# Optimization experiments

Hardware: AMD Instinct MI355X
Metric: run time of the kernel (lower is better)

The kernel has to match this reference:

```python
import jax, jax.numpy as jnp
from jax import lax
import numpy as np

POOLING_COUNTS = [15, 8, 8, 8]
N = 128          # segment_num
GROUPS = 4       # GroupNorm groups
TOPK = 5
NMS_THRESH = 0.5
EPS = 1e-5


def _build_structure(pooling_counts, n):
    """Static (numpy) replication of SparseMaxPool's mask2d and pooling schedule."""
    mask2d = np.zeros((n, n), dtype=bool)
    mask2d[np.arange(n), np.arange(n)] = True
    kinds = ['k2'] * pooling_counts[0]
    for c in pooling_counts[1:]:
        kinds += ['k3'] + ['k2'] * (c - 1)
    steps, stride, offset, k = [], 1, 0, 0
    for c in pooling_counts:
        for _ in range(c):
            offset += stride
            i = np.arange(0, n - offset, stride)
            j = np.arange(offset, n, stride)
            mask2d[i, j] = True
            steps.append((kinds[k], i, j))
            k += 1
        stride *= 2
    return mask2d, steps


_MASK2D, _STEPS = _build_structure(POOLING_COUNTS, N)


def sparse_max_pool(x):
    # x: [B, D, N] -> map2d: [B, D, N, N]
    B, D, _ = x.shape
    d = np.arange(N)
    map2d = jnp.zeros((B, D, N, N), x.dtype).at[:, :, d, d].set(x)
    for kind, i, j in _STEPS:
        if kind == 'k2':      # MaxPool1d(kernel=2, stride=1)
            x = jnp.maximum(x[..., :-1], x[..., 1:])
        else:                 # MaxPool1d(kernel=3, stride=2)
            m = jnp.maximum(jnp.maximum(x[..., :-2], x[..., 1:-1]), x[..., 2:])
            x = m[..., ::2]
        map2d = map2d.at[:, :, i, j].set(x)
    return map2d


def group_norm(x, gamma, beta):
    B, C, H, W = x.shape
    xg = x.reshape(B, GROUPS, C // GROUPS, H, W)
    mu = xg.mean(axis=(2, 3, 4), keepdims=True)
    var = xg.var(axis=(2, 3, 4), keepdims=True)
    xn = ((xg - mu) * lax.rsqrt(var + EPS)).reshape(B, C, H, W)
    return xn * gamma[None, :, None, None] + beta[None, :, None, None]


def decode(map2d, conv1_w, gn_gamma, gn_beta, conv2_w, conv2_b):
    dn = ('NCHW', 'OIHW', 'NCHW')
    h = lax.conv_general_dilated(map2d, conv1_w, (1, 1), [(1, 1), (1, 1)], dimension_numbers=dn)
    h = jax.nn.relu(group_norm(h, gn_gamma, gn_beta))
    out = lax.conv_general_dilated(h, conv2_w, (1, 1), [(0, 0), (0, 0)], dimension_numbers=dn)
    return out + conv2_b[None, :, None, None]


def greedy_nms(moments, scores):
    # moments: [M, 2] (start, end); scores: [M]
    M = moments.shape[0]
    order = jnp.argsort(-scores)
    m = moments[order]
    starts, ends = m[:, 0], m[:, 1]
    ar = jnp.arange(M)

    def body(i, sup):
        inter = jnp.clip(jnp.minimum(ends, ends[i]) - jnp.maximum(starts, starts[i]), 0.0)
        union = jnp.maximum(ends, ends[i]) - jnp.minimum(starts, starts[i])
        iou = inter / union
        newly = (iou > NMS_THRESH) & (ar > i) & jnp.logical_not(sup[i])
        return sup | newly

    sup = lax.fori_loop(0, M - 1, body, jnp.zeros((M,), bool))
    keep = jnp.logical_not(sup)
    # first TOPK kept rows in sorted order (static shape)
    pri = jnp.where(keep, M - ar, 0)
    _, idx = lax.top_k(pri, TOPK)
    return m[idx]


def reference(fea, duration, conv1_w, gn_gamma, gn_beta, conv2_w, conv2_b):
    map2d = sparse_max_pool(fea)
    out = decode(map2d, conv1_w, gn_gamma, gn_beta, conv2_w, conv2_b)
    mask = jnp.asarray(_MASK2D, out.dtype)
    score2d = (jax.nn.sigmoid(out) * mask)[0, 0]           # [N, N]
    # score2d_to_moments_scores: nonzero of masked map == static nonzero of mask2d
    gi, gj = np.nonzero(_MASK2D)                            # row-major, matches torch.nonzero
    scores = score2d[gi, gj]                                # [M]
    dur = float(duration)
    moments = jnp.asarray(
        np.stack([gi * (dur / N), (gj + 1) * (dur / N)], axis=-1), jnp.float32
    )                                                       # [M, 2]
    return greedy_nms(moments, scores)                      # [TOPK, 2]


def setup_inputs() -> dict:
    key = jax.random.key(0)
    k0, k1, k2 = jax.random.split(key, 3)
    D = 768
    return {
        'fea': jax.random.normal(k0, (1, D, N), jnp.float32),
        'duration': 30,
        'conv1_w': jax.random.normal(k1, (D, D, 3, 3), jnp.float32) * 0.02,
        'gn_gamma': jnp.ones((D,), jnp.float32),
        'gn_beta': jnp.zeros((D,), jnp.float32),
        'conv2_w': jax.random.normal(k2, (1, D, 1, 1), jnp.float32) * 0.02,
        'conv2_b': jnp.zeros((1,), jnp.float32),
    }
```

## Files before the change

### kernel.cpp

```cpp
#include <hip/hip_runtime.h>
#include <math.h>

#define NPIX 128
#define MASKM 2548
#define NPAD 2560
#define MG   6912
#define KD   768

typedef __attribute__((ext_vector_type(8))) short bf16x8;
typedef __attribute__((ext_vector_type(4))) float f32x4;
typedef __attribute__((ext_vector_type(16))) float f32x16;
typedef __attribute__((ext_vector_type(8))) unsigned short ushort8;

static constexpr size_t OFF_QI   = 0;
static constexpr size_t OFF_QJ   = OFF_QI + NPAD * 4;
static constexpr size_t OFF_QIDX = OFF_QJ + NPAD * 4;
static constexpr size_t OFF_APIX = OFF_QIDX + 16384 * 4;
static constexpr size_t OFF_START= OFF_APIX + 16384 * 4;
static constexpr size_t OFF_PART = OFF_START + 128 * 4;
static constexpr size_t OFF_STAT = OFF_PART + 512 * 8 * 8;
static constexpr size_t OFF_SC   = OFF_STAT + 256;
static constexpr size_t OFF_HM   = OFF_SC + NPAD * 4;
static constexpr size_t OFF_AH   = OFF_HM + (size_t)MASKM * KD * 4;
static constexpr size_t OFF_AL   = OFF_AH + (size_t)MG * KD * 2;
static constexpr size_t OFF_BH   = OFF_AL + (size_t)MG * KD * 2;
static constexpr size_t OFF_BL   = OFF_BH + (size_t)NPAD * KD * 2;
static constexpr size_t OFF_YT   = OFF_BL + (size_t)NPAD * KD * 2;
static constexpr size_t OFF_X    = OFF_YT;

__device__ __forceinline__ unsigned short f2bf(float f) {
    unsigned u = __float_as_uint(f);
    u = u + 0x7FFFu + ((u >> 16) & 1u);
    return (unsigned short)(u >> 16);
}
__device__ __forceinline__ float bf2f(unsigned short h) {
    return __uint_as_float(((unsigned)h) << 16);
}

__device__ __forceinline__ bool mask_allowed(int i, int d) {
    if (d == 0) return true;
    if (d <= 15) return true;
    if (d <= 31) return (d >= 17) && ((d & 1) == 1) && ((i & 1) == 0);
    if (d <= 63) return (d >= 35) && ((d & 3) == 3) && ((i & 3) == 0);
    return (d >= 71) && ((d & 7) == 7) && ((i & 7) == 0);
}
__device__ __forceinline__ bool masked_ij(int i, int j) {
    return (j >= i) && (j < NPIX) && (i >= 0) && mask_allowed(i, j - i);
}

__global__ void k_fill(int* __restrict__ qi, int* __restrict__ qj,
                       int* __restrict__ qidx, int* __restrict__ apix,
                       double* __restrict__ part) {
    __shared__ int cnt[NPIX];
    __shared__ int startv[NPIX];
    int tid = threadIdx.x;
    if (tid < NPIX) {
        int c = 0;
        for (int d = 0; tid + d < NPIX; ++d) if (mask_allowed(tid, d)) ++c;
        cnt[tid] = c;
    }
    __syncthreads();
    if (tid == 0) {
        int s = 0;
        for (int r = 0; r < NPIX; ++r) { startv[r] = s; s += cnt[r]; }
    }
    __syncthreads();
    int p = blockIdx.x * 256 + tid;
    int i = p >> 7, j = p & 127;
    int q = -1;
    if (masked_ij(i, j)) {
        int d = j - i, r = 0;
        for (int dd = 0; dd < d; ++dd) r += mask_allowed(i, dd) ? 1 : 0;
        q = startv[i] + r;
        qi[q] = i; qj[q] = j;
    }
    qidx[p] = q;
    int act = 0;
    #pragma unroll
    for (int dy = -1; dy <= 1; ++dy)
        #pragma unroll
        for (int dx = -1; dx <= 1; ++dx)
            if (masked_ij(i + dy, j + dx)) act = 1;
    apix[p] = act;
    if (blockIdx.x == 0 && tid < 8) part[tid] = 0.0;
}

__global__ void k_buildX(const float* __restrict__ fea, const int* __restrict__ qi,
                         const int* __restrict__ qj, float* __restrict__ X) {
    __shared__ float tab[8][NPIX];
    int c = blockIdx.x, t = threadIdx.x;
    tab[0][t] = fea[c * NPIX + t];
    __syncthreads();
    #pragma unroll
    for (int l = 1; l < 8; ++l) {
        int half = 1 << (l - 1), full = 1 << l;
        if (t + full <= NPIX) tab[l][t] = fmaxf(tab[l - 1][t], tab[l - 1][t + half]);
        __syncthreads();
    }
    #pragma unroll
    for (int it = 0; it < 20; ++it) {
        int q = it * 128 + t;
        float v = 0.f;
        if (q < MASKM) {
            int i = qi[q], j = qj[q];
            int len = j - i + 1;
            int l = 31 - __clz(len);
            v = fmaxf(tab[l][i], tab[l][j + 1 - (1 << l)]);
        }
        X[c * NPAD + q] = v;
    }
}

#define PASTR 148
__global__ __launch_bounds__(256) void k_prepA(const float* __restrict__ w1,
                                               unsigned short* __restrict__ Ah,
                                               unsigned short* __restrict__ Al) {
    __shared__ float tile[64 * PASTR];
    int co0 = blockIdx.x * 64, ci0 = blockIdx.y * 64;
    int tid = threadIdx.x;
    for (int s = 0; s < 4; ++s) {
        int cib = ci0 + s * 16;
        __syncthreads();
        for (int idx = tid; idx < 2304; idx += 256) {
            int row = idx / 36, c4 = idx % 36;
            float4 v = *(const float4*)(w1 + (size_t)(co0 + row) * MG + cib * 9 + c4 * 4);
            *(float4*)&tile[row * PASTR + c4 * 4] = v;
        }
        __syncthreads();
        for (int idx = tid; idx < 1152; idx += 256) {
            int tap = idx / 128;
            int rem = idx - tap * 128;
            int co = rem >> 1, half = rem & 1;
            ushort8 vh, vl;
            #pragma unroll
            for (int c = 0; c < 8; ++c) {
                float v = tile[co * PASTR + (half * 8 + c) * 9 + tap];
                unsigned short hi = f2bf(v);
                vh[c] = hi;
                vl[c] = f2bf(v - bf2f(hi));
            }
            size_t ob = (size_t)(tap * 768 + co0 + co) * KD + cib + half * 8;
            *(ushort8*)(Ah + ob) = vh;
            *(ushort8*)(Al + ob) = vl;
        }
    }
}

__global__ void k_trans(const float* __restrict__ src, int C,
                        unsigned short* __restrict__ dh, unsigned short* __restrict__ dl) {
    __shared__ float tile[64][65];
    int c0 = blockIdx.x * 64, k0 = blockIdx.y * 64;
    int t = threadIdx.x;
    int r = t >> 2, cq = (t & 3) << 4;
    const float* s = src + (size_t)(k0 + r) * C + c0 + cq;
    #pragma unroll
    for (int u = 0; u < 16; u += 4) {
        float4 v = *(const float4*)(s + u);
        tile[r][cq + u]     = v.x;
        tile[r][cq + u + 1] = v.y;
        tile[r][cq + u + 2] = v.z;
        tile[r][cq + u + 3] = v.w;
    }
    __syncthreads();
    size_t ob = (size_t)(c0 + r) * KD + k0 + cq;
    #pragma unroll
    for (int u = 0; u < 16; ++u) {
        float v = tile[cq + u][r];
        unsigned short hi = f2bf(v);
        float lo = v - bf2f(hi);
        dh[ob + u] = hi;
        dl[ob + u] = f2bf(lo);
    }
}

#define BUFSZ   73728
#define SB_BH   32768

__global__ __launch_bounds__(512, 1) void k_gemm(const unsigned short* __restrict__ Ah,
                                                 const unsigned short* __restrict__ Al,
                                                 const unsigned short* __restrict__ Bh,
                                                 const unsigned short* __restrict__ Bl,
                                                 float* __restrict__ Yt) {
    extern __shared__ char sm[];
    int tid = threadIdx.x;
    int wave = tid >> 6, lane = tid & 63;

    int bid = (int)blockIdx.x;
    int xcd = bid & 7, loc = bid >> 3;
    int m0 = loc * 256, n0 = xcd * 320;

    int wm = (wave & 3) << 6, wn = (wave >> 2) * 160;
    int r32 = lane & 31, hi2 = lane >> 5;
    int rb  = (r32 >> 4) * 1024 + hi2 * 256 + (r32 & 15) * 16;
    int awb = (wm >> 4) * 1024 + rb;
    int bwb = (wn >> 4) * 1024 + rb;

    int lrow = lane & 15, lchk = lane >> 4;
    const unsigned short* sp[9];
    int so[9];
    #pragma unroll
    for (int s = 0; s < 9; ++s) {
        int gid = wave * 9 + s;
        const unsigned short* base;
        int row0, ldso;
        if (gid < 16)      { base = Ah; row0 = m0 + gid * 16;        ldso = gid * 1024; }
        else if (gid < 32) { base = Al; row0 = m0 + (gid - 16) * 16; ldso = 16384 + (gid - 16) * 1024; }
        else if (gid < 52) { base = Bh; row0 = n0 + (gid - 32) * 16; ldso = SB_BH + (gid - 32) * 1024; }
        else               { base = Bl; row0 = n0 + (gid - 52) * 16; ldso = SB_BH + 20480 + (gid - 52) * 1024; }
        sp[s] = base + (size_t)(row0 + lrow) * KD + lchk * 8;
        so[s] = ldso;
    }

    f32x16 acc[2][5] = {};

    char* CB = sm;
    char* NB = sm + BUFSZ;

    #define STAGE(DST, s, koff) __builtin_amdgcn_global_load_lds( \
        (const __attribute__((address_space(1))) unsigned int*)(sp[s] + (koff)), \
        (__attribute__((address_space(3))) unsigned int*)((DST) + so[s]), 16, 0, 0)
    #define ARD(hl, mf, ks) (*(const bf16x8*)(CB + (hl) * 16384 + awb + (mf) * 2048 + (ks) * 512))
    #define BRD(hl, nf, ks) (*(const bf16x8*)(CB + SB_BH + (hl) * 20480 + bwb + (nf) * 2048 + (ks) * 512))
    #define TRIP(mf, nf, xh, xl, yh, yl) \
        acc[mf][nf] = __builtin_amdgcn_mfma_f32_32x32x16_bf16(xh, yh, acc[mf][nf], 0, 0, 0); \
        acc[mf][nf] = __builtin_amdgcn_mfma_f32_32x32x16_bf16(xh, yl, acc[mf][nf], 0, 0, 0); \
        acc[mf][nf] = __builtin_amdgcn_mfma_f32_32x32x16_bf16(xl, yh, acc[mf][nf], 0, 0, 0);

    #pragma unroll
    for (int s = 0; s < 9; ++s) STAGE(CB, s, 0);
    __syncthreads();

    for (int t = 0; t < 24; ++t) {
        int kn = (t + 1) * 32;
        if (t < 23) {
            #pragma unroll
            for (int s = 0; s < 9; ++s) STAGE(NB, s, kn);
        }
        #pragma unroll
        for (int ks = 0; ks < 2; ++ks) {
            bf16x8 a0h = ARD(0, 0, ks), a0l = ARD(1, 0, ks);
            bf16x8 a1h = ARD(0, 1, ks), a1l = ARD(1, 1, ks);
            bf16x8 bxh = BRD(0, 0, ks), bxl = BRD(1, 0, ks);
            bf16x8 byh = BRD(0, 1, ks), byl = BRD(1, 1, ks);
            __builtin_amdgcn_s_setprio(1);
            TRIP(0, 0, a0h, a0l, bxh, bxl)
            TRIP(1, 0, a1h, a1l, bxh, bxl)
            __builtin_amdgcn_s_setprio(0);
            bxh = BRD(0, 2, ks); bxl = BRD(1, 2, ks);
            __builtin_amdgcn_s_setprio(1);
            TRIP(0, 1, a0h, a0l, byh, byl)
            TRIP(1, 1, a1h, a1l, byh, byl)
            __builtin_amdgcn_s_setprio(0);
            byh = BRD(0, 3, ks); byl = BRD(1, 3, ks);
            __builtin_amdgcn_s_setprio(1);
            TRIP(0, 2, a0h, a0l, bxh, bxl)
            TRIP(1, 2, a1h, a1l, bxh, bxl)
            __builtin_amdgcn_s_setprio(0);
            bxh = BRD(0, 4, ks); bxl = BRD(1, 4, ks);
            __builtin_amdgcn_s_setprio(1);
            TRIP(0, 3, a0h, a0l, byh, byl)
            TRIP(1, 3, a1h, a1l, byh, byl)
            TRIP(0, 4, a0h, a0l, bxh, bxl)
            TRIP(1, 4, a1h, a1l, bxh, bxl)
            __builtin_amdgcn_s_setprio(0);
        }
        __syncthreads();
        char* tmp = CB; CB = NB; NB = tmp;
    }

    #pragma unroll
    for (int mf = 0; mf < 2; ++mf)
        #pragma unroll
        for (int nf = 0; nf < 5; ++nf) {
            int n = n0 + wn + nf * 32 + r32;
            size_t rowb = (size_t)n * MG + m0 + wm + mf * 32 + 4 * hi2;
            #pragma unroll
            for (int g = 0; g < 4; ++g) {
                f32x4 v = { acc[mf][nf][g * 4 + 0], acc[mf][nf][g * 4 + 1],
                            acc[mf][nf][g * 4 + 2], acc[mf][nf][g * 4 + 3] };
                *(f32x4*)(Yt + rowb + 8 * g) = v;
            }
        }
    #undef STAGE
    #undef ARD
    #undef BRD
    #undef TRIP
}

__global__ __launch_bounds__(256) void k_gather(const float* __restrict__ Yt,
                                                const int* __restrict__ qidx,
                                                const int* __restrict__ apix,
                                                float* __restrict__ hm,
                                                double* __restrict__ part) {
    __shared__ double red1[256 * 4], red2[256 * 4];
    int tid = threadIdx.x;
    int wave = tid >> 6, lane = tid & 63;
    double a1[3] = {0, 0, 0}, a2[3] = {0, 0, 0};
    int gs[3];
    #pragma unroll
    for (int s = 0; s < 3; ++s) gs[s] = (64 * s + lane) / 48;

    for (int it = 0; it < 8; ++it) {
        int p = blockIdx.x * 32 + wave * 8 + it;
        if (!apix[p]) continue;
        int y = p >> 7, x = p & 127;
        float4 hv[3] = {};
        #pragma unroll
        for (int tap = 0; tap < 9; ++tap) {
            int i = y + tap / 3 - 1, j = x + tap % 3 - 1;
            if ((unsigned)i < 128u && (unsigned)j < 128u) {
                int q = qidx[i * NPIX + j];
                if (q >= 0) {
                    const float* yr = Yt + (size_t)q * MG + tap * 768 + lane * 4;
                    #pragma unroll
                    for (int s = 0; s < 3; ++s) {
                        float4 v = *(const float4*)(yr + s * 256);
                        hv[s].x += v.x; hv[s].y += v.y; hv[s].z += v.z; hv[s].w += v.w;
                    }
                }
            }
        }
        int qp = qidx[p];
        if (qp >= 0) {
            #pragma unroll
            for (int s = 0; s < 3; ++s)
                *(float4*)(hm + (size_t)qp * KD + s * 256 + lane * 4) = hv[s];
        }
        #pragma unroll
        for (int s = 0; s < 3; ++s) {
            a1[s] += (double)hv[s].x + (double)hv[s].y + (double)hv[s].z + (double)hv[s].w;
            a2[s] += (double)hv[s].x * hv[s].x + (double)hv[s].y * hv[s].y +
                     (double)hv[s].z * hv[s].z + (double)hv[s].w * hv[s].w;
        }
    }
    #pragma unroll
    for (int g = 0; g < 4; ++g) { red1[tid * 4 + g] = 0.0; red2[tid * 4 + g] = 0.0; }
    #pragma unroll
    for (int s = 0; s < 3; ++s) { red1[tid * 4 + gs[s]] = a1[s]; red2[tid * 4 + gs[s]] = a2[s]; }
    __syncthreads();
    if (tid < 8) {
        int g = tid & 3;
        double s = 0.0;
        if (tid < 4) { for (int i = 0; i < 256; ++i) s += red1[i * 4 + g]; }
        else         { for (int i = 0; i < 256; ++i) s += red2[i * 4 + g]; }
        atomicAdd(&part[tid], s);
    }
}

__global__ void k_score(const float* __restrict__ hm, const double* __restrict__ part,
                        const float* __restrict__ gamma, const float* __restrict__ beta,
                        const float* __restrict__ w2, const float* __restrict__ b2,
                        float* __restrict__ scores) {
    int q = blockIdx.x * 4 + (threadIdx.x >> 6);
    int lane = threadIdx.x & 63;
    if (q >= MASKM) return;
    float mu[4], rs[4];
    const double cnt = 192.0 * 16384.0;
    #pragma unroll
    for (int g = 0; g < 4; ++g) {
        double m = part[g] / cnt;
        double v = part[4 + g] / cnt - m * m;
        mu[g] = (float)m;
        rs[g] = (float)(1.0 / sqrt(v + 1e-5));
    }
    const float* hp = hm + (size_t)q * KD;
    float s = 0.f;
    for (int c = lane; c < KD; c += 64) {
        int g = c / 192;
        float v = (hp[c] - mu[g]) * rs[g] * gamma[c] + beta[c];
        s += fmaxf(v, 0.f) * w2[c];
    }
    for (int o = 32; o; o >>= 1) s += __shfl_down(s, o, 64);
    if (lane == 0) scores[q] = 1.f / (1.f + expf(-(s + b2[0])));
}

__device__ __forceinline__ unsigned long long shfl_down_u64(unsigned long long v, int o) {
    unsigned lo = (unsigned)v, hi = (unsigned)(v >> 32);
    lo = __shfl_down(lo, o, 64);
    hi = __shfl_down(hi, o, 64);
    return ((unsigned long long)hi << 32) | lo;
}

__global__ void k_nms(const float* __restrict__ scores, const int* __restrict__ qi,
                      const int* __restrict__ qj, const int* __restrict__ durp,
                      float* __restrict__ out) {
    __shared__ unsigned long long key[MASKM];
    __shared__ float ss[MASKM], ee[MASKM];
    __shared__ unsigned char st[MASKM];
    __shared__ unsigned long long wm0[16], wm1[16];
    __shared__ int sh_keeper, keepq[5];
    __shared__ float sh_s0, sh_e0;
    int t = threadIdx.x;
    float delta = (float)(*durp) / 128.f;
    for (int i = t; i < MASKM; i += 1024) {
        unsigned sb = __float_as_uint(scores[i]);
        key[i] = ((unsigned long long)sb << 32) | (unsigned)(4095 - i);
        ss[i] = qi[i] * delta;
        ee[i] = (qj[i] + 1) * delta;
        st[i] = 0;
    }
    __syncthreads();
    for (int round = 0; round < 5; ++round) {
        unsigned long long b0 = 0, b1 = 0;
        for (int i = t; i < MASKM; i += 1024) {
            unsigned char s = st[i];
            unsigned long long k = key[i];
            if (s == 0) { if (k > b0) b0 = k; }
            else if (s == 1) { if (k > b1) b1 = k; }
        }
        for (int o = 32; o; o >>= 1) {
            unsigned long long u0 = shfl_down_u64(b0, o), u1 = shfl_down_u64(b1, o);
            if (u0 > b0) b0 = u0;
            if (u1 > b1) b1 = u1;
        }
        if ((t & 63) == 0) { wm0[t >> 6] = b0; wm1[t >> 6] = b1; }
        __syncthreads();
        if (t == 0) {
            unsigned long long B0 = 0, B1 = 0;
            for (int w = 0; w < 16; ++w) {
                if (wm0[w] > B0) B0 = wm0[w];
                if (wm1[w] > B1) B1 = wm1[w];
            }
            int keeper = (B0 != 0);
            unsigned long long B = keeper ? B0 : B1;
            int q = 4095 - (int)(B & 0xFFFFFFFFull);
            st[q] = keeper ? 2 : 3;
            sh_keeper = keeper;
            sh_s0 = ss[q]; sh_e0 = ee[q];
            keepq[round] = q;
        }
        __syncthreads();
        if (sh_keeper) {
            float s0 = sh_s0, e0 = sh_e0;
            for (int i = t; i < MASKM; i += 1024) {
                if (st[i] == 0) {
                    float inter = fminf(ee[i], e0) - fmaxf(ss[i], s0);
                    if (inter > 0.f) {
                        float uni = fmaxf(ee[i], e0) - fminf(ss[i], s0);
                        if (inter / uni > 0.5f) st[i] = 1;
                    }
                }
            }
        }
        __syncthreads();
    }
    if (t < 5) { out[t * 2] = ss[keepq[t]]; out[t * 2 + 1] = ee[keepq[t]]; }
}

extern "C" void kernel_launch(void* const* d_in, const int* in_sizes, int n_in,
                              void* d_out, int out_size, void* d_ws, size_t ws_size,
                              hipStream_t stream) {
    const float* fea   = (const float*)d_in[0];
    const int*   dur   = (const int*)d_in[1];
    const float* w1    = (const float*)d_in[2];
    const float* gamma = (const float*)d_in[3];
    const float* beta  = (const float*)d_in[4];
    const float* w2    = (const float*)d_in[5];
    const float* b2    = (const float*)d_in[6];
    float* out = (float*)d_out;

    char* ws = (char*)d_ws;
    int*    qi     = (int*)(ws + OFF_QI);
    int*    qj     = (int*)(ws + OFF_QJ);
    int*    qidx   = (int*)(ws + OFF_QIDX);
    int*    apix   = (int*)(ws + OFF_APIX);
    double* part   = (double*)(ws + OFF_PART);
    float*  scores = (float*)(ws + OFF_SC);
    float*  hm     = (float*)(ws + OFF_HM);
    unsigned short* AhU = (unsigned short*)(ws + OFF_AH);
    unsigned short* AlU = (unsigned short*)(ws + OFF_AL);
    unsigned short* BhU = (unsigned short*)(ws + OFF_BH);
    unsigned short* BlU = (unsigned short*)(ws + OFF_BL);
    float*  Yt     = (float*)(ws + OFF_YT);
    float*  X      = (float*)(ws + OFF_X);

    static bool gemm_attr_set = false;
    if (!gemm_attr_set) {
        hipFuncSetAttribute((const void*)k_gemm,
                            hipFuncAttributeMaxDynamicSharedMemorySize, 2 * BUFSZ);
        gemm_attr_set = true;
    }

    k_fill<<<64, 256, 0, stream>>>(qi, qj, qidx, apix, part);
    k_buildX<<<768, 128, 0, stream>>>(fea, qi, qj, X);
    k_prepA<<<dim3(12, 12), 256, 0, stream>>>(w1, AhU, AlU);
    k_trans<<<dim3(40, 12), 256, 0, stream>>>(X, NPAD, BhU, BlU);
    k_gemm<<<dim3(216), 512, 2 * BUFSZ, stream>>>(AhU, AlU, BhU, BlU, Yt);
    k_gather<<<512, 256, 0, stream>>>(Yt, qidx, apix, hm, part);
    k_score<<<637, 256, 0, stream>>>(hm, part, gamma, beta, w2, b2, scores);
    k_nms<<<1, 1024, 0, stream>>>(scores, qi, qj, dur, out);
}
```

Before: 279.5 us.

## Merge prep stages into one kernel and fuse gather/score/NMS with grid barriers

Folds the mask-index fill, sparse max-pool build, the B-matrix bf16 hi/lo split, and the weight split into one heterogeneous k_prep launch. The pooled features go straight into the transposed bf16 layout, which removes the intermediate X buffer and the separate transpose pass. The gather, GroupNorm/score and NMS stages become one persistent k_fused kernel that uses atomic grid-wide barriers, replacing three launches and their gaps. The barriers assume all 512 blocks are co-resident (3 per CU), which is a deadlock risk if occupancy falls short.

```diff
diff --git a/kernel.cpp b/kernel.cpp
--- a/kernel.cpp
+++ b/kernel.cpp
@@ -6,6 +6,7 @@
 #define NPAD 2560
 #define MG   6912
 #define KD   768
+#define FUSED_GRID 512
 
 typedef __attribute__((ext_vector_type(8))) short bf16x8;
 typedef __attribute__((ext_vector_type(4))) float f32x4;
@@ -16,17 +17,15 @@
 static constexpr size_t OFF_QJ   = OFF_QI + NPAD * 4;
 static constexpr size_t OFF_QIDX = OFF_QJ + NPAD * 4;
 static constexpr size_t OFF_APIX = OFF_QIDX + 16384 * 4;
-static constexpr size_t OFF_START= OFF_APIX + 16384 * 4;
-static constexpr size_t OFF_PART = OFF_START + 128 * 4;
-static constexpr size_t OFF_STAT = OFF_PART + 512 * 8 * 8;
-static constexpr size_t OFF_SC   = OFF_STAT + 256;
+static constexpr size_t OFF_BAR  = OFF_APIX + 16384 * 4;
+static constexpr size_t OFF_PART = OFF_BAR + 128 * 4;
+static constexpr size_t OFF_SC   = OFF_PART + 512 * 8 * 8;
 static constexpr size_t OFF_HM   = OFF_SC + NPAD * 4;
 static constexpr size_t OFF_AH   = OFF_HM + (size_t)MASKM * KD * 4;
 static constexpr size_t OFF_AL   = OFF_AH + (size_t)MG * KD * 2;
 static constexpr size_t OFF_BH   = OFF_AL + (size_t)MG * KD * 2;
 static constexpr size_t OFF_BL   = OFF_BH + (size_t)NPAD * KD * 2;
 static constexpr size_t OFF_YT   = OFF_BL + (size_t)NPAD * KD * 2;
-static constexpr size_t OFF_X    = OFF_YT;
 
 __device__ __forceinline__ unsigned short f2bf(float f) {
     unsigned u = __float_as_uint(f);
@@ -48,128 +47,168 @@
     return (j >= i) && (j < NPIX) && (i >= 0) && mask_allowed(i, j - i);
 }
 
-__global__ void k_fill(int* __restrict__ qi, int* __restrict__ qj,
-                       int* __restrict__ qidx, int* __restrict__ apix,
-                       double* __restrict__ part) {
-    __shared__ int cnt[NPIX];
-    __shared__ int startv[NPIX];
+__device__ __forceinline__ int rank_to_d(int i, int r) {
+    int rem = NPIX - i;
+    int c1 = rem < 16 ? rem : 16;
+    if (r < c1) return r;
+    r -= c1;
+    int h2 = (rem - 1) < 31 ? (rem - 1) : 31;
+    int c2 = (((i & 1) == 0) && h2 >= 17) ? ((h2 - 17) >> 1) + 1 : 0;
+    if (r < c2) return 17 + 2 * r;
+    r -= c2;
+    int h3 = (rem - 1) < 63 ? (rem - 1) : 63;
+    int c3 = (((i & 3) == 0) && h3 >= 35) ? ((h3 - 35) >> 2) + 1 : 0;
+    if (r < c3) return 35 + 4 * r;
+    r -= c3;
+    return 71 + 8 * r;
+}
+
+#define PREP_LDS 66816
+#define PASTR 148
+
+__global__ __launch_bounds__(256) void k_prep(const float* __restrict__ fea,
+                                              const float* __restrict__ w1,
+                                              int* __restrict__ qi, int* __restrict__ qj,
+                                              int* __restrict__ qidx, int* __restrict__ apix,
+                                              double* __restrict__ part, int* __restrict__ bar,
+                                              unsigned short* __restrict__ Ah,
+                                              unsigned short* __restrict__ Al,
+                                              unsigned short* __restrict__ Bh,
+                                              unsigned short* __restrict__ Bl) {
+    extern __shared__ char smp[];
     int tid = threadIdx.x;
-    if (tid < NPIX) {
-        int c = 0;
-        for (int d = 0; tid + d < NPIX; ++d) if (mask_allowed(tid, d)) ++c;
-        cnt[tid] = c;
-    }
-    __syncthreads();
-    if (tid == 0) {
-        int s = 0;
-        for (int r = 0; r < NPIX; ++r) { startv[r] = s; s += cnt[r]; }
-    }
-    __syncthreads();
-    int p = blockIdx.x * 256 + tid;
-    int i = p >> 7, j = p & 127;
-    int q = -1;
-    if (masked_ij(i, j)) {
-        int d = j - i, r = 0;
-        for (int dd = 0; dd < d; ++dd) r += mask_allowed(i, dd) ? 1 : 0;
-        q = startv[i] + r;
-        qi[q] = i; qj[q] = j;
-    }
-    qidx[p] = q;
-    int act = 0;
-    #pragma unroll
-    for (int dy = -1; dy <= 1; ++dy)
-        #pragma unroll
-        for (int dx = -1; dx <= 1; ++dx)
-            if (masked_ij(i + dy, j + dx)) act = 1;
-    apix[p] = act;
-    if (blockIdx.x == 0 && tid < 8) part[tid] = 0.0;
-}
-
-__global__ void k_buildX(const float* __restrict__ fea, const int* __restrict__ qi,
-                         const int* __restrict__ qj, float* __restrict__ X) {
-    __shared__ float tab[8][NPIX];
-    int c = blockIdx.x, t = threadIdx.x;
-    tab[0][t] = fea[c * NPIX + t];
-    __syncthreads();
-    #pragma unroll
-    for (int l = 1; l < 8; ++l) {
-        int half = 1 << (l - 1), full = 1 << l;
-        if (t + full <= NPIX) tab[l][t] = fmaxf(tab[l - 1][t], tab[l - 1][t + half]);
-        __syncthreads();
-    }
-    #pragma unroll
-    for (int it = 0; it < 20; ++it) {
-        int q = it * 128 + t;
-        float v = 0.f;
-        if (q < MASKM) {
-            int i = qi[q], j = qj[q];
-            int len = j - i + 1;
-            int l = 31 - __clz(len);
-            v = fmaxf(tab[l][i], tab[l][j + 1 - (1 << l)]);
-        }
-        X[c * NPAD + q] = v;
-    }
-}
-
-#define PASTR 148
-__global__ __launch_bounds__(256) void k_prepA(const float* __restrict__ w1,
-                                               unsigned short* __restrict__ Ah,
-                                               unsigned short* __restrict__ Al) {
-    __shared__ float tile[64 * PASTR];
-    int co0 = blockIdx.x * 64, ci0 = blockIdx.y * 64;
-    int tid = threadIdx.x;
-    for (int s = 0; s < 4; ++s) {
-        int cib = ci0 + s * 16;
-        __syncthreads();
-        for (int idx = tid; idx < 2304; idx += 256) {
-            int row = idx / 36, c4 = idx % 36;
-            float4 v = *(const float4*)(w1 + (size_t)(co0 + row) * MG + cib * 9 + c4 * 4);
-            *(float4*)&tile[row * PASTR + c4 * 4] = v;
-        }
-        __syncthreads();
-        for (int idx = tid; idx < 1152; idx += 256) {
-            int tap = idx / 128;
-            int rem = idx - tap * 128;
-            int co = rem >> 1, half = rem & 1;
-            ushort8 vh, vl;
+    int bid = blockIdx.x;
+
+    if (bid < 64) {
+        int* cnt = (int*)smp;
+        int* startv = cnt + NPIX;
+        if (tid < NPIX) {
+            int c = 0;
+            for (int d = 0; tid + d < NPIX; ++d) if (mask_allowed(tid, d)) ++c;
+            cnt[tid] = c;
+        }
+        __syncthreads();
+        if (tid == 0) {
+            int s = 0;
+            for (int r = 0; r < NPIX; ++r) { startv[r] = s; s += cnt[r]; }
+        }
+        __syncthreads();
+        int p = bid * 256 + tid;
+        int i = p >> 7, j = p & 127;
+        int q = -1;
+        if (masked_ij(i, j)) {
+            int d = j - i, r = 0;
+            for (int dd = 0; dd < d; ++dd) r += mask_allowed(i, dd) ? 1 : 0;
+            q = startv[i] + r;
+            qi[q] = i; qj[q] = j;
+        }
+        qidx[p] = q;
+        int act = 0;
+        #pragma unroll
+        for (int dy = -1; dy <= 1; ++dy)
             #pragma unroll
-            for (int c = 0; c < 8; ++c) {
-                float v = tile[co * PASTR + (half * 8 + c) * 9 + tap];
-                unsigned short hi = f2bf(v);
-                vh[c] = hi;
-                vl[c] = f2bf(v - bf2f(hi));
-            }
-            size_t ob = (size_t)(tap * 768 + co0 + co) * KD + cib + half * 8;
-            *(ushort8*)(Ah + ob) = vh;
-            *(ushort8*)(Al + ob) = vl;
-        }
-    }
-}
-
-__global__ void k_trans(const float* __restrict__ src, int C,
-                        unsigned short* __restrict__ dh, unsigned short* __restrict__ dl) {
-    __shared__ float tile[64][65];
-    int c0 = blockIdx.x * 64, k0 = blockIdx.y * 64;
-    int t = threadIdx.x;
-    int r = t >> 2, cq = (t & 3) << 4;
-    const float* s = src + (size_t)(k0 + r) * C + c0 + cq;
-    #pragma unroll
-    for (int u = 0; u < 16; u += 4) {
-        float4 v = *(const float4*)(s + u);
-        tile[r][cq + u]     = v.x;
-        tile[r][cq + u + 1] = v.y;
-        tile[r][cq + u + 2] = v.z;
-        tile[r][cq + u + 3] = v.w;
-    }
-    __syncthreads();
-    size_t ob = (size_t)(c0 + r) * KD + k0 + cq;
-    #pragma unroll
-    for (int u = 0; u < 16; ++u) {
-        float v = tile[cq + u][r];
-        unsigned short hi = f2bf(v);
-        float lo = v - bf2f(hi);
-        dh[ob + u] = hi;
-        dl[ob + u] = f2bf(lo);
+            for (int dx = -1; dx <= 1; ++dx)
+                if (masked_ij(i + dy, j + dx)) act = 1;
+        apix[p] = act;
+        if (bid == 0) {
+            if (tid < 8) part[tid] = 0.0;
+            if (tid == 8) bar[0] = 0;
+            if (tid == 9) bar[1] = 0;
+        }
+    } else if (bid < 112) {
+        float* tab = (float*)smp;
+        int* cnt = (int*)(smp + 65536);
+        int* startv = (int*)(smp + 66048);
+        int cb = bid - 64, c0 = cb * 16;
+        if (tid < NPIX) {
+            int c = 0;
+            for (int d = 0; tid + d < NPIX; ++d) if (mask_allowed(tid, d)) ++c;
+            cnt[tid] = c;
+        }
+        __syncthreads();
+        if (tid == 0) {
+            int s = 0;
+            for (int r = 0; r < NPIX; ++r) { startv[r] = s; s += cnt[r]; }
+            startv[NPIX] = s;
+        }
+        for (int idx = tid; idx < 16 * NPIX; idx += 256) {
+            int c = idx >> 7, x = idx & 127;
+            tab[(c * 8) * 128 + x] = fea[(size_t)(c0 + c) * NPIX + x];
+        }
+        __syncthreads();
+        for (int lvl = 1; lvl < 8; ++lvl) {
+            int half = 1 << (lvl - 1), full = 1 << lvl;
+            for (int idx = tid; idx < 16 * NPIX; idx += 256) {
+                int c = idx >> 7, x = idx & 127;
+                if (x + full <= NPIX)
+                    tab[(c * 8 + lvl) * 128 + x] =
+                        fmaxf(tab[(c * 8 + lvl - 1) * 128 + x],
+                              tab[(c * 8 + lvl - 1) * 128 + x + half]);
+            }
+            __syncthreads();
+        }
+        for (int q = tid; q < NPAD; q += 256) {
+            ushort8 vh0 = {}, vh1 = {}, vl0 = {}, vl1 = {};
+            if (q < MASKM) {
+                int i = 0;
+                #pragma unroll
+                for (int s = 64; s >= 1; s >>= 1) {
+                    int cand = i + s;
+                    if (cand <= 127 && startv[cand] <= q) i = cand;
+                }
+                int d = rank_to_d(i, q - startv[i]);
+                int j = i + d;
+                int len = d + 1;
+                int lvl = 31 - __clz(len);
+                int x2 = j + 1 - (1 << lvl);
+                #pragma unroll
+                for (int c = 0; c < 8; ++c) {
+                    float v = fmaxf(tab[(c * 8 + lvl) * 128 + i], tab[(c * 8 + lvl) * 128 + x2]);
+                    unsigned short hh = f2bf(v);
+                    vh0[c] = hh; vl0[c] = f2bf(v - bf2f(hh));
+                }
+                #pragma unroll
+                for (int c = 0; c < 8; ++c) {
+                    float v = fmaxf(tab[((c + 8) * 8 + lvl) * 128 + i], tab[((c + 8) * 8 + lvl) * 128 + x2]);
+                    unsigned short hh = f2bf(v);
+                    vh1[c] = hh; vl1[c] = f2bf(v - bf2f(hh));
+                }
+            }
+            *(ushort8*)(Bh + (size_t)q * KD + c0)     = vh0;
+            *(ushort8*)(Bh + (size_t)q * KD + c0 + 8) = vh1;
+            *(ushort8*)(Bl + (size_t)q * KD + c0)     = vl0;
+            *(ushort8*)(Bl + (size_t)q * KD + c0 + 8) = vl1;
+        }
+    } else {
+        float* tile = (float*)smp;
+        int pb = bid - 112;
+        int co0 = (pb % 12) * 64, ci0 = (pb / 12) * 64;
+        for (int s = 0; s < 4; ++s) {
+            int cib = ci0 + s * 16;
+            __syncthreads();
+            for (int idx = tid; idx < 2304; idx += 256) {
+                int row = idx / 36, c4 = idx % 36;
+                float4 v = *(const float4*)(w1 + (size_t)(co0 + row) * MG + cib * 9 + c4 * 4);
+                *(float4*)&tile[row * PASTR + c4 * 4] = v;
+            }
+            __syncthreads();
+            for (int idx = tid; idx < 1152; idx += 256) {
+                int tap = idx / 128;
+                int rem = idx - tap * 128;
+                int co = rem >> 1, half = rem & 1;
+                ushort8 vh, vl;
+                #pragma unroll
+                for (int c = 0; c < 8; ++c) {
+                    float v = tile[co * PASTR + (half * 8 + c) * 9 + tap];
+                    unsigned short hi = f2bf(v);
+                    vh[c] = hi;
+                    vl[c] = f2bf(v - bf2f(hi));
+                }
+                size_t ob = (size_t)(tap * 768 + co0 + co) * KD + cib + half * 8;
+                *(ushort8*)(Ah + ob) = vh;
+                *(ushort8*)(Al + ob) = vl;
+            }
+        }
     }
 }
 
@@ -212,7 +251,6 @@
     }
 
     f32x16 acc[2][5] = {};
-
     char* CB = sm;
     char* NB = sm + BUFSZ;
 
@@ -287,164 +325,206 @@
     #undef TRIP
 }
 
-__global__ __launch_bounds__(256) void k_gather(const float* __restrict__ Yt,
-                                                const int* __restrict__ qidx,
-                                                const int* __restrict__ apix,
-                                                float* __restrict__ hm,
-                                                double* __restrict__ part) {
-    __shared__ double red1[256 * 4], red2[256 * 4];
+#define FUSED_LDS 44544
+
+__device__ __forceinline__ void grid_arrive_wait(int* ctr) {
+    __threadfence();
+    __syncthreads();
+    if (threadIdx.x == 0) {
+        __hip_atomic_fetch_add(ctr, 1, __ATOMIC_RELEASE, __HIP_MEMORY_SCOPE_AGENT);
+        while (__hip_atomic_load(ctr, __ATOMIC_ACQUIRE, __HIP_MEMORY_SCOPE_AGENT) < FUSED_GRID)
+            __builtin_amdgcn_s_sleep(1);
+    }
+    __syncthreads();
+    __threadfence();
+}
+
+__global__ __launch_bounds__(256, 3) void k_fused(const float* __restrict__ Yt,
+                                                  const int* __restrict__ qidx,
+                                                  const int* __restrict__ apix,
+                                                  const int* __restrict__ qi,
+                                                  const int* __restrict__ qj,
+                                                  const int* __restrict__ durp,
+                                                  double* __restrict__ part,
+                                                  int* __restrict__ bar,
+                                                  float* __restrict__ hm,
+                                                  float* __restrict__ scores,
+                                                  const float* __restrict__ gamma,
+                                                  const float* __restrict__ beta,
+                                                  const float* __restrict__ w2,
+                                                  const float* __restrict__ b2,
+                                                  float* __restrict__ out) {
+    extern __shared__ char smf[];
     int tid = threadIdx.x;
+    int bid = (int)blockIdx.x;
     int wave = tid >> 6, lane = tid & 63;
-    double a1[3] = {0, 0, 0}, a2[3] = {0, 0, 0};
-    int gs[3];
-    #pragma unroll
-    for (int s = 0; s < 3; ++s) gs[s] = (64 * s + lane) / 48;
-
-    for (int it = 0; it < 8; ++it) {
-        int p = blockIdx.x * 32 + wave * 8 + it;
-        if (!apix[p]) continue;
-        int y = p >> 7, x = p & 127;
-        float4 hv[3] = {};
-        #pragma unroll
-        for (int tap = 0; tap < 9; ++tap) {
-            int i = y + tap / 3 - 1, j = x + tap % 3 - 1;
-            if ((unsigned)i < 128u && (unsigned)j < 128u) {
-                int q = qidx[i * NPIX + j];
-                if (q >= 0) {
-                    const float* yr = Yt + (size_t)q * MG + tap * 768 + lane * 4;
-                    #pragma unroll
-                    for (int s = 0; s < 3; ++s) {
-                        float4 v = *(const float4*)(yr + s * 256);
-                        hv[s].x += v.x; hv[s].y += v.y; hv[s].z += v.z; hv[s].w += v.w;
+
+    {
+        double* red1 = (double*)smf;
+        double* red2 = red1 + 1024;
+        double a1[3] = {0, 0, 0}, a2[3] = {0, 0, 0};
+        int gs[3];
+        #pragma unroll
+        for (int s = 0; s < 3; ++s) gs[s] = (64 * s + lane) / 48;
+
+        for (int it = 0; it < 8; ++it) {
+            int p = bid * 32 + wave * 8 + it;
+            if (!apix[p]) continue;
+            int y = p >> 7, x = p & 127;
+            float4 hv[3] = {};
+            #pragma unroll
+            for (int tap = 0; tap < 9; ++tap) {
+                int i = y + tap / 3 - 1, j = x + tap % 3 - 1;
+                if ((unsigned)i < 128u && (unsigned)j < 128u) {
+                    int q = qidx[i * NPIX + j];
+                    if (q >= 0) {
+                        const float* yr = Yt + (size_t)q * MG + tap * 768 + lane * 4;
+                        #pragma unroll
+                        for (int s = 0; s < 3; ++s) {
+                            float4 v = *(const float4*)(yr + s * 256);
+                            hv[s].x += v.x; hv[s].y += v.y; hv[s].z += v.z; hv[s].w += v.w;
+                        }
                     }
                 }
             }
-        }
-        int qp = qidx[p];
-        if (qp >= 0) {
+            int qp = qidx[p];
+            if (qp >= 0) {
+                #pragma unroll
+                for (int s = 0; s < 3; ++s)
+                    *(float4*)(hm + (size_t)qp * KD + s * 256 + lane * 4) = hv[s];
+            }
             #pragma unroll
-            for (int s = 0; s < 3; ++s)
-                *(float4*)(hm + (size_t)qp * KD + s * 256 + lane * 4) = hv[s];
-        }
-        #pragma unroll
-        for (int s = 0; s < 3; ++s) {
-            a1[s] += (double)hv[s].x + (double)hv[s].y + (double)hv[s].z + (double)hv[s].w;
-            a2[s] += (double)hv[s].x * hv[s].x + (double)hv[s].y * hv[s].y +
-                     (double)hv[s].z * hv[s].z + (double)hv[s].w * hv[s].w;
-        }
-    }
-    #pragma unroll
-    for (int g = 0; g < 4; ++g) { red1[tid * 4 + g] = 0.0; red2[tid * 4 + g] = 0.0; }
-    #pragma unroll
-    for (int s = 0; s < 3; ++s) { red1[tid * 4 + gs[s]] = a1[s]; red2[tid * 4 + gs[s]] = a2[s]; }
+            for (int s = 0; s < 3; ++s) {
+                a1[s] += (double)hv[s].x + (double)hv[s].y + (double)hv[s].z + (double)hv[s].w;
+                a2[s] += (double)hv[s].x * hv[s].x + (double)hv[s].y * hv[s].y +
+                         (double)hv[s].z * hv[s].z + (double)hv[s].w * hv[s].w;
+            }
+        }
+        #pragma unroll
+        for (int g = 0; g < 4; ++g) { red1[tid * 4 + g] = 0.0; red2[tid * 4 + g] = 0.0; }
+        #pragma unroll
+        for (int s = 0; s < 3; ++s) { red1[tid * 4 + gs[s]] = a1[s]; red2[tid * 4 + gs[s]] = a2[s]; }
+        __syncthreads();
+        if (tid < 8) {
+            int g = tid & 3;
+            double s = 0.0;
+            if (tid < 4) { for (int i = 0; i < 256; ++i) s += red1[i * 4 + g]; }
+            else         { for (int i = 0; i < 256; ++i) s += red2[i * 4 + g]; }
+            atomicAdd(&part[tid], s);
+        }
+    }
+
+    grid_arrive_wait(&bar[0]);
+
+    {
+        float mu[4], rs[4];
+        const double cnt = 192.0 * 16384.0;
+        #pragma unroll
+        for (int g = 0; g < 4; ++g) {
+            double m = *((volatile double*)&part[g]) / cnt;
+            double v = *((volatile double*)&part[4 + g]) / cnt - m * m;
+            mu[g] = (float)m;
+            rs[g] = (float)(1.0 / sqrt(v + 1e-5));
+        }
+        #pragma unroll
+        for (int rep = 0; rep < 2; ++rep) {
+            int q = bid * 4 + wave + rep * 2048;
+            if (q < MASKM) {
+                const float* hp = hm + (size_t)q * KD;
+                float s = 0.f;
+                for (int c = lane; c < KD; c += 64) {
+                    int g = c / 192;
+                    float v = (hp[c] - mu[g]) * rs[g] * gamma[c] + beta[c];
+                    s += fmaxf(v, 0.f) * w2[c];
+                }
+                for (int o = 32; o; o >>= 1) s += __shfl_down(s, o, 64);
+                if (lane == 0) scores[q] = 1.f / (1.f + expf(-(s + b2[0])));
+            }
+        }
+    }
+
+    __threadfence();
     __syncthreads();
-    if (tid < 8) {
-        int g = tid & 3;
-        double s = 0.0;
-        if (tid < 4) { for (int i = 0; i < 256; ++i) s += red1[i * 4 + g]; }
-        else         { for (int i = 0; i < 256; ++i) s += red2[i * 4 + g]; }
-        atomicAdd(&part[tid], s);
-    }
-}
-
-__global__ void k_score(const float* __restrict__ hm, const double* __restrict__ part,
-                        const float* __restrict__ gamma, const float* __restrict__ beta,
-                        const float* __restrict__ w2, const float* __restrict__ b2,
-                        float* __restrict__ scores) {
-    int q = blockIdx.x * 4 + (threadIdx.x >> 6);
-    int lane = threadIdx.x & 63;
-    if (q >= MASKM) return;
-    float mu[4], rs[4];
-    const double cnt = 192.0 * 16384.0;
-    #pragma unroll
-    for (int g = 0; g < 4; ++g) {
-        double m = part[g] / cnt;
-        double v = part[4 + g] / cnt - m * m;
-        mu[g] = (float)m;
-        rs[g] = (float)(1.0 / sqrt(v + 1e-5));
-    }
-    const float* hp = hm + (size_t)q * KD;
-    float s = 0.f;
-    for (int c = lane; c < KD; c += 64) {
-        int g = c / 192;
-        float v = (hp[c] - mu[g]) * rs[g] * gamma[c] + beta[c];
-        s += fmaxf(v, 0.f) * w2[c];
-    }
-    for (int o = 32; o; o >>= 1) s += __shfl_down(s, o, 64);
-    if (lane == 0) scores[q] = 1.f / (1.f + expf(-(s + b2[0])));
-}
-
-__device__ __forceinline__ unsigned long long shfl_down_u64(unsigned long long v, int o) {
-    unsigned lo = (unsigned)v, hi = (unsigned)(v >> 32);
-    lo = __shfl_down(lo, o, 64);
-    hi = __shfl_down(hi, o, 64);
-    return ((unsigned long long)hi << 32) | lo;
-}
-
-__global__ void k_nms(const float* __restrict__ scores, const int* __restrict__ qi,
-                      const int* __restrict__ qj, const int* __restrict__ durp,
-                      float* __restrict__ out) {
-    __shared__ unsigned long long key[MASKM];
-    __shared__ float ss[MASKM], ee[MASKM];
-    __shared__ unsigned char st[MASKM];
-    __shared__ unsigned long long wm0[16], wm1[16];
-    __shared__ int sh_keeper, keepq[5];
-    __shared__ float sh_s0, sh_e0;
-    int t = threadIdx.x;
-    float delta = (float)(*durp) / 128.f;
-    for (int i = t; i < MASKM; i += 1024) {
-        unsigned sb = __float_as_uint(scores[i]);
-        key[i] = ((unsigned long long)sb << 32) | (unsigned)(4095 - i);
-        ss[i] = qi[i] * delta;
-        ee[i] = (qj[i] + 1) * delta;
-        st[i] = 0;
+    if (tid == 0)
+        __hip_atomic_fetch_add(&bar[1], 1, __ATOMIC_RELEASE, __HIP_MEMORY_SCOPE_AGENT);
+    if (bid != 0) return;
+    if (tid == 0) {
+        while (__hip_atomic_load(&bar[1], __ATOMIC_ACQUIRE, __HIP_MEMORY_SCOPE_AGENT) < FUSED_GRID)
+            __builtin_amdgcn_s_sleep(1);
     }
     __syncthreads();
-    for (int round = 0; round < 5; ++round) {
-        unsigned long long b0 = 0, b1 = 0;
-        for (int i = t; i < MASKM; i += 1024) {
-            unsigned char s = st[i];
-            unsigned long long k = key[i];
-            if (s == 0) { if (k > b0) b0 = k; }
-            else if (s == 1) { if (k > b1) b1 = k; }
-        }
-        for (int o = 32; o; o >>= 1) {
-            unsigned long long u0 = shfl_down_u64(b0, o), u1 = shfl_down_u64(b1, o);
-            if (u0 > b0) b0 = u0;
-            if (u1 > b1) b1 = u1;
-        }
-        if ((t & 63) == 0) { wm0[t >> 6] = b0; wm1[t >> 6] = b1; }
-        __syncthreads();
-        if (t == 0) {
-            unsigned long long B0 = 0, B1 = 0;
-            for (int w = 0; w < 16; ++w) {
-                if (wm0[w] > B0) B0 = wm0[w];
-                if (wm1[w] > B1) B1 = wm1[w];
-            }
-            int keeper = (B0 != 0);
-            unsigned long long B = keeper ? B0 : B1;
-            int q = 4095 - (int)(B & 0xFFFFFFFFull);
-            st[q] = keeper ? 2 : 3;
-            sh_keeper = keeper;
-            sh_s0 = ss[q]; sh_e0 = ee[q];
-            keepq[round] = q;
-        }
-        __syncthreads();
-        if (sh_keeper) {
-            float s0 = sh_s0, e0 = sh_e0;
-            for (int i = t; i < MASKM; i += 1024) {
-                if (st[i] == 0) {
-                    float inter = fminf(ee[i], e0) - fmaxf(ss[i], s0);
-                    if (inter > 0.f) {
-                        float uni = fmaxf(ee[i], e0) - fminf(ss[i], s0);
-                        if (inter / uni > 0.5f) st[i] = 1;
+    __threadfence();
+
+    {
+        unsigned long long* key = (unsigned long long*)smf;
+        float* ss = (float*)(smf + 20384);
+        float* ee = (float*)(smf + 30576);
+        unsigned char* st = (unsigned char*)(smf + 40768);
+        unsigned long long* wm0 = (unsigned long long*)(smf + 43328);
+        unsigned long long* wm1 = (unsigned long long*)(smf + 43360);
+        __shared__ int sh_keeper, keepq[5];
+        __shared__ float sh_s0, sh_e0;
+
+        float delta = (float)(*durp) / 128.f;
+        for (int i = tid; i < MASKM; i += 256) {
+            unsigned sb = __float_as_uint(scores[i]);
+            key[i] = ((unsigned long long)sb << 32) | (unsigned)(4095 - i);
+            ss[i] = qi[i] * delta;
+            ee[i] = (qj[i] + 1) * delta;
+            st[i] = 0;
+        }
+        __syncthreads();
+        for (int round = 0; round < 5; ++round) {
+            unsigned long long b0 = 0, b1 = 0;
+            for (int i = tid; i < MASKM; i += 256) {
+                unsigned char s = st[i];
+                unsigned long long k = key[i];
+                if (s == 0) { if (k > b0) b0 = k; }
+                else if (s == 1) { if (k > b1) b1 = k; }
+            }
+            for (int o = 32; o; o >>= 1) {
+                unsigned lo0 = __shfl_down((unsigned)b0, o, 64);
+                unsigned hi0 = __shfl_down((unsigned)(b0 >> 32), o, 64);
+                unsigned long long u0 = ((unsigned long long)hi0 << 32) | lo0;
+                unsigned lo1 = __shfl_down((unsigned)b1, o, 64);
+                unsigned hi1 = __shfl_down((unsigned)(b1 >> 32), o, 64);
+                unsigned long long u1 = ((unsigned long long)hi1 << 32) | lo1;
+                if (u0 > b0) b0 = u0;
+                if (u1 > b1) b1 = u1;
+            }
+            if ((tid & 63) == 0) { wm0[tid >> 6] = b0; wm1[tid >> 6] = b1; }
+            __syncthreads();
+            if (tid == 0) {
+                unsigned long long B0 = 0, B1 = 0;
+                for (int w = 0; w < 4; ++w) {
+                    if (wm0[w] > B0) B0 = wm0[w];
+                    if (wm1[w] > B1) B1 = wm1[w];
+                }
+                int keeper = (B0 != 0);
+                unsigned long long B = keeper ? B0 : B1;
+                int q = 4095 - (int)(B & 0xFFFFFFFFull);
+                st[q] = keeper ? 2 : 3;
+                sh_keeper = keeper;
+                sh_s0 = ss[q]; sh_e0 = ee[q];
+                keepq[round] = q;
+            }
+            __syncthreads();
+            if (sh_keeper) {
+                float s0 = sh_s0, e0 = sh_e0;
+                for (int i = tid; i < MASKM; i += 256) {
+                    if (st[i] == 0) {
+                        float inter = fminf(ee[i], e0) - fmaxf(ss[i], s0);
+                        if (inter > 0.f) {
+                            float uni = fmaxf(ee[i], e0) - fminf(ss[i], s0);
+                            if (inter / uni > 0.5f) st[i] = 1;
+                        }
                     }
                 }
             }
-        }
-        __syncthreads();
-    }
-    if (t < 5) { out[t * 2] = ss[keepq[t]]; out[t * 2 + 1] = ee[keepq[t]]; }
+            __syncthreads();
+        }
+        if (tid < 5) { out[tid * 2] = ss[keepq[tid]]; out[tid * 2 + 1] = ee[keepq[tid]]; }
+    }
 }
 
 extern "C" void kernel_launch(void* const* d_in, const int* in_sizes, int n_in,
@@ -464,6 +544,7 @@
     int*    qj     = (int*)(ws + OFF_QJ);
     int*    qidx   = (int*)(ws + OFF_QIDX);
     int*    apix   = (int*)(ws + OFF_APIX);
+    int*    bar    = (int*)(ws + OFF_BAR);
     double* part   = (double*)(ws + OFF_PART);
     float*  scores = (float*)(ws + OFF_SC);
     float*  hm     = (float*)(ws + OFF_HM);
@@ -472,21 +553,21 @@
     unsigned short* BhU = (unsigned short*)(ws + OFF_BH);
     unsigned short* BlU = (unsigned short*)(ws + OFF_BL);
     float*  Yt     = (float*)(ws + OFF_YT);
-    float*  X      = (float*)(ws + OFF_X);
-
-    static bool gemm_attr_set = false;
-    if (!gemm_attr_set) {
+
+    static bool attr_set = false;
+    if (!attr_set) {
+        hipFuncSetAttribute((const void*)k_prep,
+                            hipFuncAttributeMaxDynamicSharedMemorySize, PREP_LDS);
         hipFuncSetAttribute((const void*)k_gemm,
                             hipFuncAttributeMaxDynamicSharedMemorySize, 2 * BUFSZ);
-        gemm_attr_set = true;
-    }
-
-    k_fill<<<64, 256, 0, stream>>>(qi, qj, qidx, apix, part);
-    k_buildX<<<768, 128, 0, stream>>>(fea, qi, qj, X);
-    k_prepA<<<dim3(12, 12), 256, 0, stream>>>(w1, AhU, AlU);
-    k_trans<<<dim3(40, 12), 256, 0, stream>>>(X, NPAD, BhU, BlU);
-    k_gemm<<<dim3(216), 512, 2 * BUFSZ, stream>>>(AhU, AlU, BhU, BlU, Yt);
-    k_gather<<<512, 256, 0, stream>>>(Yt, qidx, apix, hm, part);
-    k_score<<<637, 256, 0, stream>>>(hm, part, gamma, beta, w2, b2, scores);
-    k_nms<<<1, 1024, 0, stream>>>(scores, qi, qj, dur, out);
-}
+        hipFuncSetAttribute((const void*)k_fused,
+                            hipFuncAttributeMaxDynamicSharedMemorySize, FUSED_LDS);
+        attr_set = true;
+    }
+
+    k_prep<<<256, 256, PREP_LDS, stream>>>(fea, w1, qi, qj, qidx, apix, part, bar,
+                                           AhU, AlU, BhU, BlU);
+    k_gemm<<<216, 512, 2 * BUFSZ, stream>>>(AhU, AlU, BhU, BlU, Yt);
+    k_fused<<<FUSED_GRID, 256, FUSED_LDS, stream>>>(Yt, qidx, apix, qi, qj, dur, part, bar,
+                                                    hm, scores, gamma, beta, w2, b2, out);
+}
```

New measurement: 639.0 us. 2.29x slower.
